# Kernel tuning notes

Measured on AMD Instinct MI355X. Metric: run time of the kernel, lower is better.

## Reference

```python
import jax, jax.numpy as jnp
import numpy as np

EPS = 1e-8  # torch cosine_similarity eps


def setup_inputs() -> dict:
    key = jax.random.key(0)
    kq, km = jax.random.split(key)
    B, N, D = 256, 100000, 1024
    query = jax.random.normal(kq, (B, D), dtype=jnp.float32)
    memory = jax.random.normal(km, (N, D), dtype=jnp.float32)
    return {"query": query, "memory": memory, "k": 16}


def reference(query, memory, k):
    # Batched, fused version of HierarchicalMemory.retrieve():
    # cosine similarity of each query against every stored module, then top-k.
    # sim(q, m) = q.m / max(||q||*||m||, eps), matching F.cosine_similarity.
    qn = jnp.linalg.norm(query, axis=-1)          # [B]
    mn = jnp.linalg.norm(memory, axis=-1)         # [N]
    dots = jnp.einsum("bd,nd->bn", query, memory)  # [B, N]
    sims = dots / jnp.maximum(qn[:, None] * mn[None, :], EPS)
    top_vals, top_idx = jax.lax.top_k(sims, k)    # [B, k] each
    return top_vals, top_idx
```

## Files before the change

### kernel.cpp

```cpp
#include <hip/hip_runtime.h>
#include <math.h>

#define DDIM 1024
#define BQ 256
#define EPSV 1e-8f
#define CH 4
#define TPC 16
#define NCAND (CH * TPC)

typedef short bf16x8 __attribute__((ext_vector_type(8)));
typedef float f32x4 __attribute__((ext_vector_type(4)));

__device__ __forceinline__ unsigned short f2bf(float x) {
  union { float f; unsigned int u; } v;
  v.f = x;
  unsigned int lsb = (v.u >> 16) & 1u;
  v.u += 0x7fffu + lsb;
  return (unsigned short)(v.u >> 16);
}
__device__ __forceinline__ float bf2f(unsigned short b) {
  union { unsigned int u; float f; } v;
  v.u = ((unsigned int)b) << 16;
  return v.f;
}
__device__ __forceinline__ unsigned int cvtpk_bf16(float lo, float hi) {
  unsigned int r;
  asm("v_cvt_pk_bf16_f32 %0, %1, %2" : "=v"(r) : "v"(lo), "v"(hi));
  return r;
}

__global__ __launch_bounds__(256) void prep_q(const float* __restrict__ Q,
                                              unsigned short* __restrict__ Qb,
                                              float* __restrict__ qn) {
  int wave = threadIdx.x >> 6, lane = threadIdx.x & 63;
  int q = blockIdx.x * 4 + wave;
  const float4* src = (const float4*)(Q + (size_t)q * DDIM);
  int g = q >> 4, qrow = q & 15;
  float s = 0.f;
#pragma unroll
  for (int t4 = 0; t4 < 4; ++t4) {
    float4 v = src[t4 * 64 + lane];
    s += v.x * v.x + v.y * v.y + v.z * v.z + v.w * v.w;
    int k = t4 * 256 + lane * 4;
    int tt = k >> 5;
    int kquad = (k >> 3) & 3;
    int elem = k & 7;
    size_t chunk = (size_t)(tt * 16 + g) * 64 + kquad * 16 + qrow;
    ushort4 o;
    o.x = f2bf(v.x); o.y = f2bf(v.y); o.z = f2bf(v.z); o.w = f2bf(v.w);
    *(ushort4*)(Qb + chunk * 8 + elem) = o;
  }
#pragma unroll
  for (int o = 32; o > 0; o >>= 1) s += __shfl_down(s, o, 64);
  if (lane == 0) qn[q] = sqrtf(s);
}

__global__ __launch_bounds__(256) void gemm_topk(
    const float* __restrict__ M, const unsigned short* __restrict__ Qb,
    unsigned short* __restrict__ sims, int N, int Npitch) {
  __shared__ unsigned short Ms[2][64 * 32];
  __shared__ float rls[64];
  const int tid = threadIdx.x;
  const int wave = tid >> 6, lane = tid & 63;
  const int quad = lane >> 4, l15 = lane & 15;
  const int n0 = blockIdx.x * 64;

  const int mrow = tid >> 2;
  const int mchunk = tid & 3;
  const bool mvalid = (n0 + mrow) < N;
  const float* mptr = M + (size_t)(mvalid ? (n0 + mrow) : 0) * DDIM + mchunk * 8;

  const bf16x8* qptr = (const bf16x8*)Qb + (size_t)wave * 256 + lane;

  f32x4 acc[4][4];
#pragma unroll
  for (int i = 0; i < 4; ++i)
#pragma unroll
    for (int j = 0; j < 4; ++j) acc[i][j] = (f32x4){0.f, 0.f, 0.f, 0.f};
  float sumsq = 0.f;

  bf16x8 aA0 = qptr[0], aA1 = qptr[64], aA2 = qptr[128], aA3 = qptr[192];
  bf16x8 aB0{}, aB1{}, aB2{}, aB3{};
  float4 mrA0 = *(const float4*)(mptr);
  float4 mrA1 = *(const float4*)(mptr + 4);
  float4 mrB0 = *(const float4*)(mptr + 32);
  float4 mrB1 = *(const float4*)(mptr + 36);

  auto body = [&](int t, int buf, float4& r0, float4& r1, bf16x8& c0,
                  bf16x8& c1, bf16x8& c2, bf16x8& c3, bf16x8& p0, bf16x8& p1,
                  bf16x8& p2, bf16x8& p3) {
    sumsq += r0.x * r0.x + r0.y * r0.y + r0.z * r0.z + r0.w * r0.w +
             r1.x * r1.x + r1.y * r1.y + r1.z * r1.z + r1.w * r1.w;
    uint4 packed;
    packed.x = cvtpk_bf16(r0.x, r0.y);
    packed.y = cvtpk_bf16(r0.z, r0.w);
    packed.z = cvtpk_bf16(r1.x, r1.y);
    packed.w = cvtpk_bf16(r1.z, r1.w);
    *(uint4*)&Ms[buf][mrow * 32 + mchunk * 8] = packed;
    int k2 = t * 32 + 64;
    const float* p = mptr + ((k2 < DDIM) ? k2 : 0);
    r0 = *(const float4*)(p);
    r1 = *(const float4*)(p + 4);
    asm volatile("s_waitcnt lgkmcnt(0)" ::: "memory");
    __builtin_amdgcn_s_barrier();
    __builtin_amdgcn_sched_barrier(0);
    const bf16x8* qp = qptr + (size_t)((t + 1) & 31) * 1024;
    p0 = qp[0]; p1 = qp[64]; p2 = qp[128]; p3 = qp[192];
    bf16x8 bfr[4];
#pragma unroll
    for (int j = 0; j < 4; ++j)
      bfr[j] = *(const bf16x8*)&Ms[buf][(j * 16 + l15) * 32 + quad * 8];
    acc[0][0] = __builtin_amdgcn_mfma_f32_16x16x32_bf16(c0, bfr[0], acc[0][0], 0, 0, 0);
    acc[0][1] = __builtin_amdgcn_mfma_f32_16x16x32_bf16(c0, bfr[1], acc[0][1], 0, 0, 0);
    acc[0][2] = __builtin_amdgcn_mfma_f32_16x16x32_bf16(c0, bfr[2], acc[0][2], 0, 0, 0);
    acc[0][3] = __builtin_amdgcn_mfma_f32_16x16x32_bf16(c0, bfr[3], acc[0][3], 0, 0, 0);
    acc[1][0] = __builtin_amdgcn_mfma_f32_16x16x32_bf16(c1, bfr[0], acc[1][0], 0, 0, 0);
    acc[1][1] = __builtin_amdgcn_mfma_f32_16x16x32_bf16(c1, bfr[1], acc[1][1], 0, 0, 0);
    acc[1][2] = __builtin_amdgcn_mfma_f32_16x16x32_bf16(c1, bfr[2], acc[1][2], 0, 0, 0);
    acc[1][3] = __builtin_amdgcn_mfma_f32_16x16x32_bf16(c1, bfr[3], acc[1][3], 0, 0, 0);
    acc[2][0] = __builtin_amdgcn_mfma_f32_16x16x32_bf16(c2, bfr[0], acc[2][0], 0, 0, 0);
    acc[2][1] = __builtin_amdgcn_mfma_f32_16x16x32_bf16(c2, bfr[1], acc[2][1], 0, 0, 0);
    acc[2][2] = __builtin_amdgcn_mfma_f32_16x16x32_bf16(c2, bfr[2], acc[2][2], 0, 0, 0);
    acc[2][3] = __builtin_amdgcn_mfma_f32_16x16x32_bf16(c2, bfr[3], acc[2][3], 0, 0, 0);
    acc[3][0] = __builtin_amdgcn_mfma_f32_16x16x32_bf16(c3, bfr[0], acc[3][0], 0, 0, 0);
    acc[3][1] = __builtin_amdgcn_mfma_f32_16x16x32_bf16(c3, bfr[1], acc[3][1], 0, 0, 0);
    acc[3][2] = __builtin_amdgcn_mfma_f32_16x16x32_bf16(c3, bfr[2], acc[3][2], 0, 0, 0);
    acc[3][3] = __builtin_amdgcn_mfma_f32_16x16x32_bf16(c3, bfr[3], acc[3][3], 0, 0, 0);
  };

#pragma unroll 1
  for (int t = 0; t < 32; t += 2) {
    body(t, 0, mrA0, mrA1, aA0, aA1, aA2, aA3, aB0, aB1, aB2, aB3);
    body(t + 1, 1, mrB0, mrB1, aB0, aB1, aB2, aB3, aA0, aA1, aA2, aA3);
  }

  float s = sumsq;
  s += __shfl_xor(s, 1, 64);
  s += __shfl_xor(s, 2, 64);
  if (mchunk == 0) rls[mrow] = (s > 0.f) ? rsqrtf(s) : 0.f;
  __syncthreads();

#pragma unroll
  for (int j = 0; j < 4; ++j) {
    float rm = rls[j * 16 + l15];
#pragma unroll
    for (int i = 0; i < 4; ++i)
#pragma unroll
      for (int r = 0; r < 4; ++r) {
        int q = wave * 64 + i * 16 + quad * 4 + r;
        int n = n0 + j * 16 + l15;
        sims[(size_t)q * Npitch + n] = f2bf(acc[i][j][r] * rm);
      }
  }
}

__device__ __forceinline__ bool better(float v1, int i1, float v2, int i2) {
  return v1 > v2 || (v1 == v2 && i1 < i2);
}

template <int L>
__device__ __forceinline__ void insert_topL(float (&tv)[L], int (&ti)[L],
                                            float v, int idx) {
  if (v > tv[L - 1] || (v == tv[L - 1] && idx < ti[L - 1])) {
    tv[L - 1] = v; ti[L - 1] = idx;
#pragma unroll
    for (int j = L - 1; j > 0; --j) {
      if (better(tv[j], ti[j], tv[j - 1], ti[j - 1])) {
        float fv = tv[j]; tv[j] = tv[j - 1]; tv[j - 1] = fv;
        int ii = ti[j]; ti[j] = ti[j - 1]; ti[j - 1] = ii;
      }
    }
  }
}

template <int L, typename F>
__device__ __forceinline__ void block_extract(float (&tv)[L], int (&ti)[L],
                                              int rounds, F&& emit) {
  __shared__ float s_v[4];
  __shared__ int s_i[4];
  __shared__ int s_t[4];
  __shared__ float s_wv;
  __shared__ int s_wi;
  __shared__ int s_wt;
  for (int r = 0; r < rounds; ++r) {
    float v = tv[0];
    int idx = ti[0];
    int src = threadIdx.x;
#pragma unroll
    for (int o = 32; o > 0; o >>= 1) {
      float ov = __shfl_down(v, o, 64);
      int oi = __shfl_down(idx, o, 64);
      int os = __shfl_down(src, o, 64);
      if (better(ov, oi, v, idx)) { v = ov; idx = oi; src = os; }
    }
    int lane = threadIdx.x & 63, w = threadIdx.x >> 6;
    if (lane == 0) { s_v[w] = v; s_i[w] = idx; s_t[w] = src; }
    __syncthreads();
    if (threadIdx.x == 0) {
      float bv = s_v[0]; int bi = s_i[0]; int bt = s_t[0];
      for (int w2 = 1; w2 < 4; ++w2)
        if (better(s_v[w2], s_i[w2], bv, bi)) { bv = s_v[w2]; bi = s_i[w2]; bt = s_t[w2]; }
      s_wv = bv; s_wi = bi; s_wt = bt;
    }
    __syncthreads();
    if (threadIdx.x == s_wt) {
#pragma unroll
      for (int j = 0; j < L - 1; ++j) { tv[j] = tv[j + 1]; ti[j] = ti[j + 1]; }
      tv[L - 1] = -INFINITY; ti[L - 1] = 0x7fffffff;
    }
    if (threadIdx.x == 0) emit(r, s_wv, s_wi);
    __syncthreads();
  }
}

__global__ __launch_bounds__(256) void select_chunks(
    const unsigned short* __restrict__ sims, int* __restrict__ cand,
    int N, int Npitch, int Nc) {
  int q = blockIdx.y;
  int c = blockIdx.x;
  int start = c * Nc;
  int end = start + Nc;
  if (end > N) end = N;
  float tv[8]; int ti[8];
#pragma unroll
  for (int j = 0; j < 8; ++j) { tv[j] = -INFINITY; ti[j] = 0x7fffffff; }
  const unsigned short* row = sims + (size_t)q * Npitch;
  int base = start + threadIdx.x * 8;
  for (; base + 8 <= end; base += 2048) {
    uint4 wv = *(const uint4*)(row + base);
    float f0 = bf2f((unsigned short)(wv.x & 0xffff));
    float f1 = bf2f((unsigned short)(wv.x >> 16));
    float f2 = bf2f((unsigned short)(wv.y & 0xffff));
    float f3 = bf2f((unsigned short)(wv.y >> 16));
    float f4 = bf2f((unsigned short)(wv.z & 0xffff));
    float f5 = bf2f((unsigned short)(wv.z >> 16));
    float f6 = bf2f((unsigned short)(wv.w & 0xffff));
    float f7 = bf2f((unsigned short)(wv.w >> 16));
    insert_topL<8>(tv, ti, f0, base + 0);
    insert_topL<8>(tv, ti, f1, base + 1);
    insert_topL<8>(tv, ti, f2, base + 2);
    insert_topL<8>(tv, ti, f3, base + 3);
    insert_topL<8>(tv, ti, f4, base + 4);
    insert_topL<8>(tv, ti, f5, base + 5);
    insert_topL<8>(tv, ti, f6, base + 6);
    insert_topL<8>(tv, ti, f7, base + 7);
  }
  if (base < end) {
    for (int n = base; n < end; ++n)
      insert_topL<8>(tv, ti, bf2f(row[n]), n);
  }
  int* dst = cand + (size_t)q * NCAND + c * TPC;
  block_extract<8>(tv, ti, TPC, [&](int r, float v, int i) {
    dst[r] = (i == 0x7fffffff) ? 0 : i;
  });
}

__global__ __launch_bounds__(512) void rescore(
    const float* __restrict__ Q, const float* __restrict__ M,
    const float* __restrict__ qn, const int* __restrict__ cand,
    float* __restrict__ out, int N) {
  __shared__ float cosv[NCAND];
  __shared__ int cidx[NCAND];
  int q = blockIdx.x;
  int wave = threadIdx.x >> 6, lane = threadIdx.x & 63;
  const float4* qf4 = (const float4*)(Q + (size_t)q * DDIM);
  float4 qv[4];
#pragma unroll
  for (int t = 0; t < 4; ++t) qv[t] = qf4[t * 64 + lane];
  float qnv = qn[q];
#pragma unroll 1
  for (int i = 0; i < NCAND / 8; ++i) {
    int c = wave * (NCAND / 8) + i;
    int idx = cand[(size_t)q * NCAND + c];
    if (idx < 0 || idx >= N) idx = 0;
    const float4* mf4 = (const float4*)(M + (size_t)idx * DDIM);
    float dot = 0.f, sq = 0.f;
#pragma unroll
    for (int t = 0; t < 4; ++t) {
      float4 m = mf4[t * 64 + lane];
      dot += m.x * qv[t].x + m.y * qv[t].y + m.z * qv[t].z + m.w * qv[t].w;
      sq += m.x * m.x + m.y * m.y + m.z * m.z + m.w * m.w;
    }
#pragma unroll
    for (int o = 32; o > 0; o >>= 1) {
      dot += __shfl_down(dot, o, 64);
      sq += __shfl_down(sq, o, 64);
    }
    if (lane == 0) {
      cosv[c] = dot / fmaxf(qnv * sqrtf(sq), EPSV);
      cidx[c] = idx;
    }
  }
  __syncthreads();
  if (wave == 0) {
    float v0 = cosv[lane];
    int i0 = cidx[lane];
    for (int r = 0; r < 16; ++r) {
      float bv = v0;
      int bi = i0;
      int bs = lane;
#pragma unroll
      for (int o = 32; o > 0; o >>= 1) {
        float ov = __shfl_down(bv, o, 64);
        int oi = __shfl_down(bi, o, 64);
        int os = __shfl_down(bs, o, 64);
        if (better(ov, oi, bv, bi)) { bv = ov; bi = oi; bs = os; }
      }
      bv = __shfl(bv, 0, 64);
      bi = __shfl(bi, 0, 64);
      bs = __shfl(bs, 0, 64);
      if (lane == bs) v0 = -INFINITY;
      if (lane == 0) {
        out[(size_t)q * 16 + r] = bv;
        out[(size_t)BQ * 16 + (size_t)q * 16 + r] = (float)bi;
      }
    }
  }
}

extern "C" void kernel_launch(void* const* d_in, const int* in_sizes, int n_in,
                              void* d_out, int out_size, void* d_ws, size_t ws_size,
                              hipStream_t stream) {
  const float* Q = (const float*)d_in[0];
  const float* M = (const float*)d_in[1];
  int N = in_sizes[1] / DDIM;
  float* out = (float*)d_out;

  int nb = (N + 63) / 64;
  int Npitch = nb * 64;

  char* w = (char*)d_ws;
  size_t off = 0;
  auto alloc = [&](size_t bytes) {
    char* p = w + off;
    off = (off + bytes + 255) & ~(size_t)255;
    return p;
  };
  unsigned short* Qb = (unsigned short*)alloc((size_t)BQ * DDIM * 2);
  float* qn = (float*)alloc((size_t)BQ * 4);
  int* cand = (int*)alloc((size_t)BQ * NCAND * 4);
  unsigned short* sims = (unsigned short*)alloc((size_t)BQ * Npitch * 2);
  (void)ws_size;

  int Nc = (((N + CH - 1) / CH) + 7) & ~7;

  prep_q<<<BQ / 4, 256, 0, stream>>>(Q, Qb, qn);
  gemm_topk<<<nb, 256, 0, stream>>>(M, Qb, sims, N, Npitch);
  select_chunks<<<dim3(CH, BQ), 256, 0, stream>>>(sims, cand, N, Npitch, Nc);
  rescore<<<BQ, 512, 0, stream>>>(Q, M, qn, cand, out, N);
}
```

Measured before the change: 676.3 us.

## Widen GEMM tile to 128 memory rows and add early-skip in top-k scan

```diff
diff --git a/kernel.cpp b/kernel.cpp
--- a/kernel.cpp
+++ b/kernel.cpp
@@ -55,93 +55,128 @@
   if (lane == 0) qn[q] = sqrtf(s);
 }
 
-__global__ __launch_bounds__(256) void gemm_topk(
+__global__ __launch_bounds__(256, 2) void gemm_topk(
     const float* __restrict__ M, const unsigned short* __restrict__ Qb,
     unsigned short* __restrict__ sims, int N, int Npitch) {
-  __shared__ unsigned short Ms[2][64 * 32];
-  __shared__ float rls[64];
+  __shared__ unsigned short Ms[2][128 * 32];
+  __shared__ float rls[128];
   const int tid = threadIdx.x;
   const int wave = tid >> 6, lane = tid & 63;
   const int quad = lane >> 4, l15 = lane & 15;
-  const int n0 = blockIdx.x * 64;
-
-  const int mrow = tid >> 2;
-  const int mchunk = tid & 3;
+  const int n0 = blockIdx.x * 128;
+
+  const int mrow = tid >> 1;
+  const int mc = (tid & 1) * 16;
   const bool mvalid = (n0 + mrow) < N;
-  const float* mptr = M + (size_t)(mvalid ? (n0 + mrow) : 0) * DDIM + mchunk * 8;
+  const float* mptr = M + (size_t)(mvalid ? (n0 + mrow) : 0) * DDIM + mc;
 
   const bf16x8* qptr = (const bf16x8*)Qb + (size_t)wave * 256 + lane;
 
-  f32x4 acc[4][4];
+  f32x4 acc[4][8];
 #pragma unroll
   for (int i = 0; i < 4; ++i)
 #pragma unroll
-    for (int j = 0; j < 4; ++j) acc[i][j] = (f32x4){0.f, 0.f, 0.f, 0.f};
+    for (int j = 0; j < 8; ++j) acc[i][j] = (f32x4){0.f, 0.f, 0.f, 0.f};
   float sumsq = 0.f;
 
   bf16x8 aA0 = qptr[0], aA1 = qptr[64], aA2 = qptr[128], aA3 = qptr[192];
   bf16x8 aB0{}, aB1{}, aB2{}, aB3{};
   float4 mrA0 = *(const float4*)(mptr);
   float4 mrA1 = *(const float4*)(mptr + 4);
+  float4 mrA2 = *(const float4*)(mptr + 8);
+  float4 mrA3 = *(const float4*)(mptr + 12);
   float4 mrB0 = *(const float4*)(mptr + 32);
   float4 mrB1 = *(const float4*)(mptr + 36);
-
-  auto body = [&](int t, int buf, float4& r0, float4& r1, bf16x8& c0,
-                  bf16x8& c1, bf16x8& c2, bf16x8& c3, bf16x8& p0, bf16x8& p1,
-                  bf16x8& p2, bf16x8& p3) {
+  float4 mrB2 = *(const float4*)(mptr + 40);
+  float4 mrB3 = *(const float4*)(mptr + 44);
+
+  auto body = [&](int t, int buf, float4& r0, float4& r1, float4& r2,
+                  float4& r3, bf16x8& c0, bf16x8& c1, bf16x8& c2, bf16x8& c3,
+                  bf16x8& p0, bf16x8& p1, bf16x8& p2, bf16x8& p3) {
     sumsq += r0.x * r0.x + r0.y * r0.y + r0.z * r0.z + r0.w * r0.w +
-             r1.x * r1.x + r1.y * r1.y + r1.z * r1.z + r1.w * r1.w;
-    uint4 packed;
-    packed.x = cvtpk_bf16(r0.x, r0.y);
-    packed.y = cvtpk_bf16(r0.z, r0.w);
-    packed.z = cvtpk_bf16(r1.x, r1.y);
-    packed.w = cvtpk_bf16(r1.z, r1.w);
-    *(uint4*)&Ms[buf][mrow * 32 + mchunk * 8] = packed;
+             r1.x * r1.x + r1.y * r1.y + r1.z * r1.z + r1.w * r1.w +
+             r2.x * r2.x + r2.y * r2.y + r2.z * r2.z + r2.w * r2.w +
+             r3.x * r3.x + r3.y * r3.y + r3.z * r3.z + r3.w * r3.w;
+    uint4 pk0, pk1;
+    pk0.x = cvtpk_bf16(r0.x, r0.y);
+    pk0.y = cvtpk_bf16(r0.z, r0.w);
+    pk0.z = cvtpk_bf16(r1.x, r1.y);
+    pk0.w = cvtpk_bf16(r1.z, r1.w);
+    pk1.x = cvtpk_bf16(r2.x, r2.y);
+    pk1.y = cvtpk_bf16(r2.z, r2.w);
+    pk1.z = cvtpk_bf16(r3.x, r3.y);
+    pk1.w = cvtpk_bf16(r3.z, r3.w);
+    *(uint4*)&Ms[buf][mrow * 32 + mc] = pk0;
+    *(uint4*)&Ms[buf][mrow * 32 + mc + 8] = pk1;
     int k2 = t * 32 + 64;
     const float* p = mptr + ((k2 < DDIM) ? k2 : 0);
     r0 = *(const float4*)(p);
     r1 = *(const float4*)(p + 4);
+    r2 = *(const float4*)(p + 8);
+    r3 = *(const float4*)(p + 12);
     asm volatile("s_waitcnt lgkmcnt(0)" ::: "memory");
     __builtin_amdgcn_s_barrier();
     __builtin_amdgcn_sched_barrier(0);
     const bf16x8* qp = qptr + (size_t)((t + 1) & 31) * 1024;
     p0 = qp[0]; p1 = qp[64]; p2 = qp[128]; p3 = qp[192];
-    bf16x8 bfr[4];
-#pragma unroll
-    for (int j = 0; j < 4; ++j)
-      bfr[j] = *(const bf16x8*)&Ms[buf][(j * 16 + l15) * 32 + quad * 8];
-    acc[0][0] = __builtin_amdgcn_mfma_f32_16x16x32_bf16(c0, bfr[0], acc[0][0], 0, 0, 0);
-    acc[0][1] = __builtin_amdgcn_mfma_f32_16x16x32_bf16(c0, bfr[1], acc[0][1], 0, 0, 0);
-    acc[0][2] = __builtin_amdgcn_mfma_f32_16x16x32_bf16(c0, bfr[2], acc[0][2], 0, 0, 0);
-    acc[0][3] = __builtin_amdgcn_mfma_f32_16x16x32_bf16(c0, bfr[3], acc[0][3], 0, 0, 0);
-    acc[1][0] = __builtin_amdgcn_mfma_f32_16x16x32_bf16(c1, bfr[0], acc[1][0], 0, 0, 0);
-    acc[1][1] = __builtin_amdgcn_mfma_f32_16x16x32_bf16(c1, bfr[1], acc[1][1], 0, 0, 0);
-    acc[1][2] = __builtin_amdgcn_mfma_f32_16x16x32_bf16(c1, bfr[2], acc[1][2], 0, 0, 0);
-    acc[1][3] = __builtin_amdgcn_mfma_f32_16x16x32_bf16(c1, bfr[3], acc[1][3], 0, 0, 0);
-    acc[2][0] = __builtin_amdgcn_mfma_f32_16x16x32_bf16(c2, bfr[0], acc[2][0], 0, 0, 0);
-    acc[2][1] = __builtin_amdgcn_mfma_f32_16x16x32_bf16(c2, bfr[1], acc[2][1], 0, 0, 0);
-    acc[2][2] = __builtin_amdgcn_mfma_f32_16x16x32_bf16(c2, bfr[2], acc[2][2], 0, 0, 0);
-    acc[2][3] = __builtin_amdgcn_mfma_f32_16x16x32_bf16(c2, bfr[3], acc[2][3], 0, 0, 0);
-    acc[3][0] = __builtin_amdgcn_mfma_f32_16x16x32_bf16(c3, bfr[0], acc[3][0], 0, 0, 0);
-    acc[3][1] = __builtin_amdgcn_mfma_f32_16x16x32_bf16(c3, bfr[1], acc[3][1], 0, 0, 0);
-    acc[3][2] = __builtin_amdgcn_mfma_f32_16x16x32_bf16(c3, bfr[2], acc[3][2], 0, 0, 0);
-    acc[3][3] = __builtin_amdgcn_mfma_f32_16x16x32_bf16(c3, bfr[3], acc[3][3], 0, 0, 0);
+    {
+      bf16x8 bfr0 = *(const bf16x8*)&Ms[buf][(0 * 16 + l15) * 32 + quad * 8];
+      bf16x8 bfr1 = *(const bf16x8*)&Ms[buf][(1 * 16 + l15) * 32 + quad * 8];
+      bf16x8 bfr2 = *(const bf16x8*)&Ms[buf][(2 * 16 + l15) * 32 + quad * 8];
+      bf16x8 bfr3 = *(const bf16x8*)&Ms[buf][(3 * 16 + l15) * 32 + quad * 8];
+      acc[0][0] = __builtin_amdgcn_mfma_f32_16x16x32_bf16(c0, bfr0, acc[0][0], 0, 0, 0);
+      acc[0][1] = __builtin_amdgcn_mfma_f32_16x16x32_bf16(c0, bfr1, acc[0][1], 0, 0, 0);
+      acc[0][2] = __builtin_amdgcn_mfma_f32_16x16x32_bf16(c0, bfr2, acc[0][2], 0, 0, 0);
+      acc[0][3] = __builtin_amdgcn_mfma_f32_16x16x32_bf16(c0, bfr3, acc[0][3], 0, 0, 0);
+      acc[1][0] = __builtin_amdgcn_mfma_f32_16x16x32_bf16(c1, bfr0, acc[1][0], 0, 0, 0);
+      acc[1][1] = __builtin_amdgcn_mfma_f32_16x16x32_bf16(c1, bfr1, acc[1][1], 0, 0, 0);
+      acc[1][2] = __builtin_amdgcn_mfma_f32_16x16x32_bf16(c1, bfr2, acc[1][2], 0, 0, 0);
+      acc[1][3] = __builtin_amdgcn_mfma_f32_16x16x32_bf16(c1, bfr3, acc[1][3], 0, 0, 0);
+      acc[2][0] = __builtin_amdgcn_mfma_f32_16x16x32_bf16(c2, bfr0, acc[2][0], 0, 0, 0);
+      acc[2][1] = __builtin_amdgcn_mfma_f32_16x16x32_bf16(c2, bfr1, acc[2][1], 0, 0, 0);
+      acc[2][2] = __builtin_amdgcn_mfma_f32_16x16x32_bf16(c2, bfr2, acc[2][2], 0, 0, 0);
+      acc[2][3] = __builtin_amdgcn_mfma_f32_16x16x32_bf16(c2, bfr3, acc[2][3], 0, 0, 0);
+      acc[3][0] = __builtin_amdgcn_mfma_f32_16x16x32_bf16(c3, bfr0, acc[3][0], 0, 0, 0);
+      acc[3][1] = __builtin_amdgcn_mfma_f32_16x16x32_bf16(c3, bfr1, acc[3][1], 0, 0, 0);
+      acc[3][2] = __builtin_amdgcn_mfma_f32_16x16x32_bf16(c3, bfr2, acc[3][2], 0, 0, 0);
+      acc[3][3] = __builtin_amdgcn_mfma_f32_16x16x32_bf16(c3, bfr3, acc[3][3], 0, 0, 0);
+    }
+    {
+      bf16x8 bfr4 = *(const bf16x8*)&Ms[buf][(4 * 16 + l15) * 32 + quad * 8];
+      bf16x8 bfr5 = *(const bf16x8*)&Ms[buf][(5 * 16 + l15) * 32 + quad * 8];
+      bf16x8 bfr6 = *(const bf16x8*)&Ms[buf][(6 * 16 + l15) * 32 + quad * 8];
+      bf16x8 bfr7 = *(const bf16x8*)&Ms[buf][(7 * 16 + l15) * 32 + quad * 8];
+      acc[0][4] = __builtin_amdgcn_mfma_f32_16x16x32_bf16(c0, bfr4, acc[0][4], 0, 0, 0);
+      acc[0][5] = __builtin_amdgcn_mfma_f32_16x16x32_bf16(c0, bfr5, acc[0][5], 0, 0, 0);
+      acc[0][6] = __builtin_amdgcn_mfma_f32_16x16x32_bf16(c0, bfr6, acc[0][6], 0, 0, 0);
+      acc[0][7] = __builtin_amdgcn_mfma_f32_16x16x32_bf16(c0, bfr7, acc[0][7], 0, 0, 0);
+      acc[1][4] = __builtin_amdgcn_mfma_f32_16x16x32_bf16(c1, bfr4, acc[1][4], 0, 0, 0);
+      acc[1][5] = __builtin_amdgcn_mfma_f32_16x16x32_bf16(c1, bfr5, acc[1][5], 0, 0, 0);
+      acc[1][6] = __builtin_amdgcn_mfma_f32_16x16x32_bf16(c1, bfr6, acc[1][6], 0, 0, 0);
+      acc[1][7] = __builtin_amdgcn_mfma_f32_16x16x32_bf16(c1, bfr7, acc[1][7], 0, 0, 0);
+      acc[2][4] = __builtin_amdgcn_mfma_f32_16x16x32_bf16(c2, bfr4, acc[2][4], 0, 0, 0);
+      acc[2][5] = __builtin_amdgcn_mfma_f32_16x16x32_bf16(c2, bfr5, acc[2][5], 0, 0, 0);
+      acc[2][6] = __builtin_amdgcn_mfma_f32_16x16x32_bf16(c2, bfr6, acc[2][6], 0, 0, 0);
+      acc[2][7] = __builtin_amdgcn_mfma_f32_16x16x32_bf16(c2, bfr7, acc[2][7], 0, 0, 0);
+      acc[3][4] = __builtin_amdgcn_mfma_f32_16x16x32_bf16(c3, bfr4, acc[3][4], 0, 0, 0);
+      acc[3][5] = __builtin_amdgcn_mfma_f32_16x16x32_bf16(c3, bfr5, acc[3][5], 0, 0, 0);
+      acc[3][6] = __builtin_amdgcn_mfma_f32_16x16x32_bf16(c3, bfr6, acc[3][6], 0, 0, 0);
+      acc[3][7] = __builtin_amdgcn_mfma_f32_16x16x32_bf16(c3, bfr7, acc[3][7], 0, 0, 0);
+    }
   };
 
 #pragma unroll 1
   for (int t = 0; t < 32; t += 2) {
-    body(t, 0, mrA0, mrA1, aA0, aA1, aA2, aA3, aB0, aB1, aB2, aB3);
-    body(t + 1, 1, mrB0, mrB1, aB0, aB1, aB2, aB3, aA0, aA1, aA2, aA3);
-  }
-
-  float s = sumsq;
-  s += __shfl_xor(s, 1, 64);
-  s += __shfl_xor(s, 2, 64);
-  if (mchunk == 0) rls[mrow] = (s > 0.f) ? rsqrtf(s) : 0.f;
+    body(t, 0, mrA0, mrA1, mrA2, mrA3, aA0, aA1, aA2, aA3, aB0, aB1, aB2, aB3);
+    body(t + 1, 1, mrB0, mrB1, mrB2, mrB3, aB0, aB1, aB2, aB3, aA0, aA1, aA2, aA3);
+  }
+
+  float s = sumsq + __shfl_xor(sumsq, 1, 64);
+  if ((tid & 1) == 0) rls[mrow] = (s > 0.f) ? rsqrtf(s) : 0.f;
   __syncthreads();
 
 #pragma unroll
-  for (int j = 0; j < 4; ++j) {
+  for (int j = 0; j < 8; ++j) {
     float rm = rls[j * 16 + l15];
 #pragma unroll
     for (int i = 0; i < 4; ++i)
@@ -236,14 +271,18 @@
     float f5 = bf2f((unsigned short)(wv.z >> 16));
     float f6 = bf2f((unsigned short)(wv.w & 0xffff));
     float f7 = bf2f((unsigned short)(wv.w >> 16));
-    insert_topL<8>(tv, ti, f0, base + 0);
-    insert_topL<8>(tv, ti, f1, base + 1);
-    insert_topL<8>(tv, ti, f2, base + 2);
-    insert_topL<8>(tv, ti, f3, base + 3);
-    insert_topL<8>(tv, ti, f4, base + 4);
-    insert_topL<8>(tv, ti, f5, base + 5);
-    insert_topL<8>(tv, ti, f6, base + 6);
-    insert_topL<8>(tv, ti, f7, base + 7);
+    float mx = fmaxf(fmaxf(fmaxf(f0, f1), fmaxf(f2, f3)),
+                     fmaxf(fmaxf(f4, f5), fmaxf(f6, f7)));
+    if (mx > tv[7]) {
+      insert_topL<8>(tv, ti, f0, base + 0);
+      insert_topL<8>(tv, ti, f1, base + 1);
+      insert_topL<8>(tv, ti, f2, base + 2);
+      insert_topL<8>(tv, ti, f3, base + 3);
+      insert_topL<8>(tv, ti, f4, base + 4);
+      insert_topL<8>(tv, ti, f5, base + 5);
+      insert_topL<8>(tv, ti, f6, base + 6);
+      insert_topL<8>(tv, ti, f7, base + 7);
+    }
   }
   if (base < end) {
     for (int n = base; n < end; ++n)
@@ -326,8 +365,8 @@
   int N = in_sizes[1] / DDIM;
   float* out = (float*)d_out;
 
-  int nb = (N + 63) / 64;
-  int Npitch = nb * 64;
+  int nb = (N + 127) / 128;
+  int Npitch = nb * 128;
 
   char* w = (char*)d_ws;
   size_t off = 0;
```

After: 682.2 us. No clear change (+0.9%).
